# Kernel tuning notes

Hardware: AMD Instinct MI355X
Metric: run time of the kernel (lower is better)

Reference implementation:

```python
import jax, jax.numpy as jnp
import numpy as np

D_MODEL = 256
N_HEADS = 8
D_K = D_MODEL // N_HEADS
D_HID = D_MODEL // 2
LN_EPS = 1e-5


def setup_inputs() -> dict:
    key = jax.random.key(0)
    ks = jax.random.split(key, 16)
    B, ND, NT = 4, 512, 512
    s = 1.0 / np.sqrt(D_MODEL)
    inp = {
        'detections': jax.random.normal(ks[0], (B, ND, D_MODEL), jnp.float32),
        'tracks': jax.random.normal(ks[1], (B, NT, D_MODEL), jnp.float32),
        # attention projections, torch Linear convention: W [out, in], y = x W^T + b
        'w_q': jax.random.normal(ks[2], (D_MODEL, D_MODEL), jnp.float32) * s,
        'b_q': jnp.zeros((D_MODEL,), jnp.float32),
        'w_k': jax.random.normal(ks[3], (D_MODEL, D_MODEL), jnp.float32) * s,
        'b_k': jnp.zeros((D_MODEL,), jnp.float32),
        'w_v': jax.random.normal(ks[4], (D_MODEL, D_MODEL), jnp.float32) * s,
        'b_v': jnp.zeros((D_MODEL,), jnp.float32),
        'w_o': jax.random.normal(ks[5], (D_MODEL, D_MODEL), jnp.float32) * s,
        'b_o': jnp.zeros((D_MODEL,), jnp.float32),
        # LayerNorm
        'ln_g': jnp.ones((D_MODEL,), jnp.float32),
        'ln_b': jnp.zeros((D_MODEL,), jnp.float32),
        # association head MLP
        'w1': jax.random.normal(ks[6], (D_HID, D_MODEL), jnp.float32) * s,
        'b1': jnp.zeros((D_HID,), jnp.float32),
        'w2': jax.random.normal(ks[7], (1, D_HID), jnp.float32) * (1.0 / np.sqrt(D_HID)),
        'b2': jnp.zeros((1,), jnp.float32),
    }
    return inp


def _forward(detections, tracks, w_q, b_q, w_k, b_k, w_v, b_v, w_o, b_o,
             ln_g, ln_b, w1, b1, w2, b2):
    B, ND, D = detections.shape
    NT = tracks.shape[1]
    # cross-attention: query=detections, key=value=tracks
    Q = (detections @ w_q.T + b_q).reshape(B, ND, N_HEADS, D_K).transpose(0, 2, 1, 3)
    K = (tracks @ w_k.T + b_k).reshape(B, NT, N_HEADS, D_K).transpose(0, 2, 1, 3)
    V = (tracks @ w_v.T + b_v).reshape(B, NT, N_HEADS, D_K).transpose(0, 2, 1, 3)
    scores = jnp.einsum('bhqd,bhkd->bhqk', Q, K) / np.sqrt(D_K)
    attn = jax.nn.softmax(scores, axis=-1)
    ctx = jnp.einsum('bhqk,bhkd->bhqd', attn, V)  # [B,H,ND,D_K]
    ctx = ctx.transpose(0, 2, 1, 3).reshape(B, ND, D)
    attended = ctx @ w_o.T + b_o
    # residual + LayerNorm (dropout = identity in eval)
    x = detections + attended
    mu = jnp.mean(x, axis=-1, keepdims=True)
    var = jnp.var(x, axis=-1, keepdims=True)
    xn = (x - mu) * jax.lax.rsqrt(var + LN_EPS) * ln_g + ln_b
    # pairwise broadcast-multiply + 2-layer MLP + sigmoid
    combined = xn[:, :, None, :] * tracks[:, None, :, :]  # [B,ND,NT,D]
    h = jax.nn.relu(jnp.einsum('bntd,hd->bnth', combined, w1) + b1)
    logits = jnp.einsum('bnth,oh->bnto', h, w2) + b2  # [B,ND,NT,1]
    return jax.nn.sigmoid(logits[..., 0])


def reference(detections, tracks, w_q, b_q, w_k, b_k, w_v, b_v, w_o, b_o,
              ln_g, ln_b, w1, b1, w2, b2):
    return _forward(detections, tracks, w_q, b_q, w_k, b_k, w_v, b_v, w_o, b_o,
                    ln_g, ln_b, w1, b1, w2, b2)
```

## Files before the change

### kernel.cpp

```cpp
#include <hip/hip_runtime.h>

typedef _Float16 half8 __attribute__((ext_vector_type(8)));
typedef _Float16 half4v __attribute__((ext_vector_type(4)));
typedef _Float16 half2v __attribute__((ext_vector_type(2)));
typedef float f32x4 __attribute__((ext_vector_type(4)));

struct CvtJobs {
    const float* src[7];
    _Float16* dst[7];
    int n[7];
};

__global__ __launch_bounds__(256) void cvt_kernel(CvtJobs j) {
    int job = blockIdx.y;
    const float* s = j.src[job];
    _Float16* d = j.dst[job];
    int n = j.n[job];
    for (int i = blockIdx.x * blockDim.x + threadIdx.x; i < n;
         i += gridDim.x * blockDim.x)
        d[i] = (_Float16)s[i];
}

template<int MODE>
__global__ __launch_bounds__(256) void gemm_tn(
    const _Float16* __restrict__ A, const _Float16* __restrict__ Bm,
    _Float16* __restrict__ Ch, float* __restrict__ Cf,
    const float* __restrict__ bias, float alpha,
    int M, int N, int K, int lda, int ldb, int ldc)
{
    __shared__ _Float16 As[64][40];
    __shared__ _Float16 Bs[64][40];

    int tid = threadIdx.x;
    int l = tid & 63, w = tid >> 6;
    int wm = (w >> 1) * 32, wn = (w & 1) * 32;
    int m0 = blockIdx.x * 64, n0 = blockIdx.y * 64;
    int lr = tid >> 2, lc = (tid & 3) * 8;
    int ko = (l >> 4) * 8;

    f32x4 acc[2][2]{};

    for (int k0 = 0; k0 < K; k0 += 32) {
        half8 av = *(const half8*)(A + (long)(m0 + lr) * lda + k0 + lc);
        half8 bv = *(const half8*)(Bm + (long)(n0 + lr) * ldb + k0 + lc);
        __syncthreads();
        *(half8*)(&As[lr][lc]) = av;
        *(half8*)(&Bs[lr][lc]) = bv;
        __syncthreads();
        half8 a0 = *(const half8*)(&As[wm + (l & 15)][ko]);
        half8 a1 = *(const half8*)(&As[wm + 16 + (l & 15)][ko]);
        half8 b0 = *(const half8*)(&Bs[wn + (l & 15)][ko]);
        half8 b1 = *(const half8*)(&Bs[wn + 16 + (l & 15)][ko]);
        acc[0][0] = __builtin_amdgcn_mfma_f32_16x16x32_f16(a0, b0, acc[0][0], 0, 0, 0);
        acc[0][1] = __builtin_amdgcn_mfma_f32_16x16x32_f16(a0, b1, acc[0][1], 0, 0, 0);
        acc[1][0] = __builtin_amdgcn_mfma_f32_16x16x32_f16(a1, b0, acc[1][0], 0, 0, 0);
        acc[1][1] = __builtin_amdgcn_mfma_f32_16x16x32_f16(a1, b1, acc[1][1], 0, 0, 0);
    }

    #pragma unroll
    for (int mm = 0; mm < 2; ++mm)
    #pragma unroll
    for (int nn = 0; nn < 2; ++nn) {
        int row  = wm + mm * 16 + (l >> 4) * 4;
        int colg = n0 + wn + nn * 16 + (l & 15);
        float bc = bias ? bias[colg] : 0.f;
        if (MODE == 2) {
            half4v hv;
            #pragma unroll
            for (int i = 0; i < 4; ++i)
                hv[i] = (_Float16)(acc[mm][nn][i] * alpha + bc);
            int grow = m0 + row;
            int bb = grow >> 9, t = grow & 511;
            long off = ((long)(bb * 8 + (colg >> 5)) * 32 + (colg & 31)) * 512 + t;
            *(half4v*)(Ch + off) = hv;
        } else if (MODE == 0) {
            #pragma unroll
            for (int i = 0; i < 4; ++i)
                Ch[(long)(m0 + row + i) * ldc + colg] =
                    (_Float16)(acc[mm][nn][i] * alpha + bc);
        } else {
            #pragma unroll
            for (int i = 0; i < 4; ++i)
                Cf[(long)(m0 + row + i) * ldc + colg] =
                    acc[mm][nn][i] * alpha + bc;
        }
    }
}

__global__ __launch_bounds__(256) void flash_kernel(
    const _Float16* __restrict__ Q, const _Float16* __restrict__ K,
    const _Float16* __restrict__ vt, _Float16* __restrict__ ctx)
{
    __shared__ _Float16 P[4][16][264];
    int bh = blockIdx.y, b = bh >> 3, h = bh & 7;
    int q0 = blockIdx.x * 64;
    int tid = threadIdx.x, l = tid & 63, w = tid >> 6;
    int l15 = l & 15, g = l >> 4;

    const _Float16* qp = Q + ((long)b * 512 + q0 + w * 16 + l15) * 256 + h * 32 + g * 8;
    half8 qf = *(const half8*)qp;
    #pragma unroll
    for (int i = 0; i < 8; ++i) qf[i] = qf[i] * (_Float16)0.17677669529663687f;

    const _Float16* kp = K + ((long)b * 512 + l15) * 256 + h * 32 + g * 8;
    const _Float16* vp = vt + ((long)bh * 32 + l15) * 512 + g * 8;

    f32x4 c0{}, c1{};
    float m_run = -3e38f, sum_run = 0.f;
    f32x4 zero{};

    #pragma unroll
    for (int hf = 0; hf < 2; ++hf) {
        f32x4 s[16];
        #pragma unroll
        for (int t = 0; t < 16; ++t) {
            half8 kf = *(const half8*)(kp + (long)(hf * 16 + t) * (16 * 256));
            s[t] = __builtin_amdgcn_mfma_f32_16x16x32_f16(kf, qf, zero, 0, 0, 0);
        }
        float m0 = -3e38f, m1 = -3e38f, m2 = -3e38f, m3 = -3e38f;
        #pragma unroll
        for (int t = 0; t < 16; ++t) {
            m0 = fmaxf(m0, s[t][0]); m1 = fmaxf(m1, s[t][1]);
            m2 = fmaxf(m2, s[t][2]); m3 = fmaxf(m3, s[t][3]);
        }
        float ml = fmaxf(fmaxf(m0, m1), fmaxf(m2, m3));
        ml = fmaxf(ml, __shfl_xor(ml, 16, 64));
        ml = fmaxf(ml, __shfl_xor(ml, 32, 64));
        float m_new = fmaxf(m_run, ml);
        float scale = __expf(m_run - m_new);
        #pragma unroll
        for (int i = 0; i < 4; ++i) { c0[i] *= scale; c1[i] *= scale; }
        sum_run *= scale;
        float s0 = 0.f, s1 = 0.f, s2 = 0.f, s3 = 0.f;
        #pragma unroll
        for (int t = 0; t < 16; ++t) {
            s[t][0] = __expf(s[t][0] - m_new); s0 += s[t][0];
            s[t][1] = __expf(s[t][1] - m_new); s1 += s[t][1];
            s[t][2] = __expf(s[t][2] - m_new); s2 += s[t][2];
            s[t][3] = __expf(s[t][3] - m_new); s3 += s[t][3];
        }
        sum_run += (s0 + s1) + (s2 + s3);
        m_run = m_new;

        #pragma unroll
        for (int t = 0; t < 16; ++t) {
            half2v p01, p23;
            p01[0] = (_Float16)s[t][0]; p01[1] = (_Float16)s[t][1];
            p23[0] = (_Float16)s[t][2]; p23[1] = (_Float16)s[t][3];
            *(half2v*)&P[w][l15][t * 16 + g * 4]     = p01;
            *(half2v*)&P[w][l15][t * 16 + g * 4 + 2] = p23;
        }
        #pragma unroll
        for (int s2i = 0; s2i < 8; ++s2i) {
            half8 bf = *(const half8*)&P[w][l15][s2i * 32 + g * 8];
            half8 a0 = *(const half8*)(vp + hf * 256 + s2i * 32);
            half8 a1 = *(const half8*)(vp + 16 * 512 + hf * 256 + s2i * 32);
            c0 = __builtin_amdgcn_mfma_f32_16x16x32_f16(a0, bf, c0, 0, 0, 0);
            c1 = __builtin_amdgcn_mfma_f32_16x16x32_f16(a1, bf, c1, 0, 0, 0);
        }
    }
    sum_run += __shfl_xor(sum_run, 16, 64);
    sum_run += __shfl_xor(sum_run, 32, 64);
    float rs = 1.f / sum_run;
    _Float16* cp = ctx + ((long)b * 512 + q0 + w * 16 + l15) * 256 + h * 32;
    #pragma unroll
    for (int i = 0; i < 4; ++i) {
        cp[g * 4 + i]      = (_Float16)(c0[i] * rs);
        cp[16 + g * 4 + i] = (_Float16)(c1[i] * rs);
    }
}

__global__ __launch_bounds__(256) void ln_kernel(
    const float* __restrict__ det, const float* __restrict__ att,
    const float* __restrict__ g, const float* __restrict__ bta,
    _Float16* __restrict__ xn)
{
    int row = blockIdx.x, tid = threadIdx.x;
    long idx = (long)row * 256 + tid;
    float x = det[idx] + att[idx];
    float s1 = x, s2 = x * x;
    #pragma unroll
    for (int off = 32; off; off >>= 1) {
        s1 += __shfl_xor(s1, off, 64);
        s2 += __shfl_xor(s2, off, 64);
    }
    __shared__ float r1[4], r2[4];
    if ((tid & 63) == 0) { r1[tid >> 6] = s1; r2[tid >> 6] = s2; }
    __syncthreads();
    float S1 = r1[0] + r1[1] + r1[2] + r1[3];
    float S2 = r2[0] + r2[1] + r2[2] + r2[3];
    float mean = S1 * (1.f / 256.f);
    float var  = S2 * (1.f / 256.f) - mean * mean;
    float rsv = rsqrtf(var + 1e-5f);
    xn[idx] = (_Float16)((x - mean) * rsv * g[tid] + bta[tid]);
}

__global__ __launch_bounds__(256) void mlp_kernel(
    const _Float16* __restrict__ xn, const _Float16* __restrict__ trk,
    const _Float16* __restrict__ w1, const float* __restrict__ w2,
    const float* __restrict__ b1, const float* __restrict__ b2,
    float* __restrict__ out)
{
    int b  = blockIdx.z;
    int n0 = blockIdx.x * 32;
    int t0 = blockIdx.y * 32;
    int tid = threadIdx.x;
    int l = tid & 63, w = tid >> 6;
    int l15 = l & 15, g = l >> 4;
    int ko = g * 8;

    __shared__ _Float16 ts[32][264];
    __shared__ float part[4][32][33];

    {
        const _Float16* src = trk + ((long)b * 512 + t0) * 256;
        int r = tid >> 3, c0s = (tid & 7) * 8;
        #pragma unroll
        for (int c = 0; c < 256; c += 64)
            *(half8*)(&ts[r][c + c0s]) = *(const half8*)(src + r * 256 + c + c0s);
    }

    half8 wf[2][8];
    {
        const _Float16* w1p = w1 + (w * 32 + l15) * 256 + ko;
        #pragma unroll
        for (int a = 0; a < 2; ++a)
            #pragma unroll
            for (int ks = 0; ks < 8; ++ks)
                wf[a][ks] = *(const half8*)(w1p + a * 16 * 256 + ks * 32);
    }
    f32x4 binit[2]; f32x4 w2v[2];
    #pragma unroll
    for (int a = 0; a < 2; ++a)
        #pragma unroll
        for (int i = 0; i < 4; ++i) {
            int hh = w * 32 + a * 16 + g * 4 + i;
            binit[a][i] = b1[hh];
            w2v[a][i]   = w2[hh];
        }

    half8 bx[2][8];
    {
        const _Float16* xb = xn + ((long)b * 512 + n0 + l15) * 256 + ko;
        #pragma unroll
        for (int mm = 0; mm < 2; ++mm)
            #pragma unroll
            for (int ks = 0; ks < 8; ++ks)
                bx[mm][ks] = *(const half8*)(xb + mm * 16 * 256 + ks * 32);
    }

    __syncthreads();

    for (int tl = 0; tl < 32; ++tl) {
        f32x4 acc[2][2];
        #pragma unroll
        for (int a = 0; a < 2; ++a) {
            acc[a][0] = binit[a];
            acc[a][1] = binit[a];
        }
        #pragma unroll
        for (int ks = 0; ks < 8; ++ks) {
            half8 tf = *(const half8*)(&ts[tl][ks * 32 + ko]);
            half8 sa0 = wf[0][ks] * tf;
            half8 sa1 = wf[1][ks] * tf;
            acc[0][0] = __builtin_amdgcn_mfma_f32_16x16x32_f16(sa0, bx[0][ks], acc[0][0], 0, 0, 0);
            acc[0][1] = __builtin_amdgcn_mfma_f32_16x16x32_f16(sa0, bx[1][ks], acc[0][1], 0, 0, 0);
            acc[1][0] = __builtin_amdgcn_mfma_f32_16x16x32_f16(sa1, bx[0][ks], acc[1][0], 0, 0, 0);
            acc[1][1] = __builtin_amdgcn_mfma_f32_16x16x32_f16(sa1, bx[1][ks], acc[1][1], 0, 0, 0);
        }
        #pragma unroll
        for (int mm = 0; mm < 2; ++mm) {
            float x = 0.f;
            #pragma unroll
            for (int a = 0; a < 2; ++a)
                #pragma unroll
                for (int i = 0; i < 4; ++i)
                    x = fmaf(fmaxf(acc[a][mm][i], 0.f), w2v[a][i], x);
            x += __shfl_xor(x, 16, 64);
            x += __shfl_xor(x, 32, 64);
            if (g == 0) part[w][tl][mm * 16 + l15] = x;
        }
    }
    __syncthreads();

    float b2v = b2[0];
    int t = tid & 31;
    int nbase = tid >> 5;
    float* op = out + ((long)b * 512 + n0) * 512 + t0;
    #pragma unroll
    for (int k = 0; k < 4; ++k) {
        int nn = nbase + k * 8;
        float s = part[0][t][nn] + part[1][t][nn]
                + part[2][t][nn] + part[3][t][nn] + b2v;
        op[(long)nn * 512 + t] = 1.f / (1.f + __expf(-s));
    }
}

extern "C" void kernel_launch(void* const* d_in, const int* in_sizes, int n_in,
                              void* d_out, int out_size, void* d_ws, size_t ws_size,
                              hipStream_t stream)
{
    const float* det  = (const float*)d_in[0];
    const float* trk  = (const float*)d_in[1];
    const float* w_q  = (const float*)d_in[2];
    const float* b_q  = (const float*)d_in[3];
    const float* w_k  = (const float*)d_in[4];
    const float* b_k  = (const float*)d_in[5];
    const float* w_v  = (const float*)d_in[6];
    const float* b_v  = (const float*)d_in[7];
    const float* w_o  = (const float*)d_in[8];
    const float* b_o  = (const float*)d_in[9];
    const float* ln_g = (const float*)d_in[10];
    const float* ln_b = (const float*)d_in[11];
    const float* w1   = (const float*)d_in[12];
    const float* b1   = (const float*)d_in[13];
    const float* w2   = (const float*)d_in[14];
    const float* b2   = (const float*)d_in[15];
    float* out = (float*)d_out;

    char* ws = (char*)d_ws;
    const size_t O_DETH = 0;
    const size_t O_TRKH = O_DETH + (size_t)1048576;
    const size_t O_WQH  = O_TRKH + (size_t)1048576;
    const size_t O_WKH  = O_WQH + 131072;
    const size_t O_WVH  = O_WKH + 131072;
    const size_t O_WOH  = O_WVH + 131072;
    const size_t O_W1H  = O_WOH + 131072;
    const size_t O_QH   = O_W1H + 65536;
    const size_t O_KH   = O_QH + (size_t)1048576;
    const size_t O_VT   = O_KH + (size_t)1048576;
    const size_t O_CTXH = O_VT + (size_t)1048576;
    const size_t O_XNH  = O_CTXH + (size_t)1048576;
    const size_t O_ATT  = O_XNH + (size_t)1048576;

    _Float16* det_h  = (_Float16*)(ws + O_DETH);
    _Float16* trk_h  = (_Float16*)(ws + O_TRKH);
    _Float16* wq_h   = (_Float16*)(ws + O_WQH);
    _Float16* wk_h   = (_Float16*)(ws + O_WKH);
    _Float16* wv_h   = (_Float16*)(ws + O_WVH);
    _Float16* wo_h   = (_Float16*)(ws + O_WOH);
    _Float16* w1_h   = (_Float16*)(ws + O_W1H);
    _Float16* Q_h    = (_Float16*)(ws + O_QH);
    _Float16* K_h    = (_Float16*)(ws + O_KH);
    _Float16* vt     = (_Float16*)(ws + O_VT);
    _Float16* ctx_h  = (_Float16*)(ws + O_CTXH);
    _Float16* xn_h   = (_Float16*)(ws + O_XNH);
    float*    att_f  = (float*)(ws + O_ATT);

    CvtJobs cj;
    cj.src[0] = det; cj.dst[0] = det_h; cj.n[0] = 2048 * 256;
    cj.src[1] = trk; cj.dst[1] = trk_h; cj.n[1] = 2048 * 256;
    cj.src[2] = w_q; cj.dst[2] = wq_h;  cj.n[2] = 65536;
    cj.src[3] = w_k; cj.dst[3] = wk_h;  cj.n[3] = 65536;
    cj.src[4] = w_v; cj.dst[4] = wv_h;  cj.n[4] = 65536;
    cj.src[5] = w_o; cj.dst[5] = wo_h;  cj.n[5] = 65536;
    cj.src[6] = w1;  cj.dst[6] = w1_h;  cj.n[6] = 32768;
    cvt_kernel<<<dim3(512, 7), 256, 0, stream>>>(cj);

    gemm_tn<0><<<dim3(32, 4), 256, 0, stream>>>(det_h, wq_h, Q_h, nullptr, b_q, 1.f,
        2048, 256, 256, 256, 256, 256);
    gemm_tn<0><<<dim3(32, 4), 256, 0, stream>>>(trk_h, wk_h, K_h, nullptr, b_k, 1.f,
        2048, 256, 256, 256, 256, 256);
    gemm_tn<2><<<dim3(32, 4), 256, 0, stream>>>(trk_h, wv_h, vt, nullptr, b_v, 1.f,
        2048, 256, 256, 256, 256, 256);
    flash_kernel<<<dim3(8, 32), 256, 0, stream>>>(Q_h, K_h, vt, ctx_h);
    gemm_tn<1><<<dim3(32, 4), 256, 0, stream>>>(ctx_h, wo_h, nullptr, att_f, b_o, 1.f,
        2048, 256, 256, 256, 256, 256);
    ln_kernel<<<2048, 256, 0, stream>>>(det, att_f, ln_g, ln_b, xn_h);
    mlp_kernel<<<dim3(16, 16, 4), 256, 0, stream>>>(xn_h, trk_h, w1_h, w2, b1, b2, out);

    (void)in_sizes; (void)n_in; (void)out_size; (void)ws_size;
}
```

Baseline: 201.0 us.

## Fuse fp32→fp16 conversion into GEMMs, merge QKV, fuse out-proj with LayerNorm, 32x32 MFMA

Drops the standalone conversion kernel and converts fp32 inputs and weights to fp16 on the fly inside each consumer. The three QKV projections become a single launch over a z grid dimension. The output projection is fused with the residual add and LayerNorm, so the fp32 attention buffer round trip goes away. The MLP kernel moves to 32x32x16 MFMA tiles. Together these cut launch count and intermediate memory traffic, but the fused out-proj/LN kernel launches only 32 blocks, which may underuse the GPU.

```diff
diff --git a/kernel.cpp b/kernel.cpp
--- a/kernel.cpp
+++ b/kernel.cpp
@@ -4,57 +4,56 @@
 typedef _Float16 half4v __attribute__((ext_vector_type(4)));
 typedef _Float16 half2v __attribute__((ext_vector_type(2)));
 typedef float f32x4 __attribute__((ext_vector_type(4)));
-
-struct CvtJobs {
-    const float* src[7];
-    _Float16* dst[7];
-    int n[7];
-};
-
-__global__ __launch_bounds__(256) void cvt_kernel(CvtJobs j) {
-    int job = blockIdx.y;
-    const float* s = j.src[job];
-    _Float16* d = j.dst[job];
-    int n = j.n[job];
-    for (int i = blockIdx.x * blockDim.x + threadIdx.x; i < n;
-         i += gridDim.x * blockDim.x)
-        d[i] = (_Float16)s[i];
-}
-
-template<int MODE>
-__global__ __launch_bounds__(256) void gemm_tn(
-    const _Float16* __restrict__ A, const _Float16* __restrict__ Bm,
-    _Float16* __restrict__ Ch, float* __restrict__ Cf,
-    const float* __restrict__ bias, float alpha,
-    int M, int N, int K, int lda, int ldb, int ldc)
-{
+typedef float f32x16 __attribute__((ext_vector_type(16)));
+
+__device__ __forceinline__ half8 cvt8(const float4 a, const float4 b) {
+    half8 r;
+    r[0] = (_Float16)a.x; r[1] = (_Float16)a.y; r[2] = (_Float16)a.z; r[3] = (_Float16)a.w;
+    r[4] = (_Float16)b.x; r[5] = (_Float16)b.y; r[6] = (_Float16)b.z; r[7] = (_Float16)b.w;
+    return r;
+}
+
+__global__ __launch_bounds__(256) void qkv_kernel(
+    const float* __restrict__ det, const float* __restrict__ trk,
+    const float* __restrict__ wq, const float* __restrict__ wk,
+    const float* __restrict__ wv, const float* __restrict__ bq,
+    const float* __restrict__ bk, const float* __restrict__ bv,
+    _Float16* __restrict__ Qh, _Float16* __restrict__ Kh,
+    _Float16* __restrict__ vt)
+{
+    int z = blockIdx.z;
+    const float* A    = (z == 0) ? det : trk;
+    const float* Bm   = (z == 0) ? wq : (z == 1) ? wk : wv;
+    const float* bias = (z == 0) ? bq : (z == 1) ? bk : bv;
+
     __shared__ _Float16 As[64][40];
     __shared__ _Float16 Bs[64][40];
 
-    int tid = threadIdx.x;
-    int l = tid & 63, w = tid >> 6;
+    int tid = threadIdx.x, l = tid & 63, w = tid >> 6;
     int wm = (w >> 1) * 32, wn = (w & 1) * 32;
     int m0 = blockIdx.x * 64, n0 = blockIdx.y * 64;
     int lr = tid >> 2, lc = (tid & 3) * 8;
-    int ko = (l >> 4) * 8;
+    int ko = (l >> 4) * 8, l15 = l & 15;
 
     f32x4 acc[2][2]{};
 
-    for (int k0 = 0; k0 < K; k0 += 32) {
-        half8 av = *(const half8*)(A + (long)(m0 + lr) * lda + k0 + lc);
-        half8 bv = *(const half8*)(Bm + (long)(n0 + lr) * ldb + k0 + lc);
+    for (int k0 = 0; k0 < 256; k0 += 32) {
+        float4 a0 = *(const float4*)(A + (long)(m0 + lr) * 256 + k0 + lc);
+        float4 a1 = *(const float4*)(A + (long)(m0 + lr) * 256 + k0 + lc + 4);
+        float4 b0 = *(const float4*)(Bm + (long)(n0 + lr) * 256 + k0 + lc);
+        float4 b1 = *(const float4*)(Bm + (long)(n0 + lr) * 256 + k0 + lc + 4);
         __syncthreads();
-        *(half8*)(&As[lr][lc]) = av;
-        *(half8*)(&Bs[lr][lc]) = bv;
+        *(half8*)&As[lr][lc] = cvt8(a0, a1);
+        *(half8*)&Bs[lr][lc] = cvt8(b0, b1);
         __syncthreads();
-        half8 a0 = *(const half8*)(&As[wm + (l & 15)][ko]);
-        half8 a1 = *(const half8*)(&As[wm + 16 + (l & 15)][ko]);
-        half8 b0 = *(const half8*)(&Bs[wn + (l & 15)][ko]);
-        half8 b1 = *(const half8*)(&Bs[wn + 16 + (l & 15)][ko]);
-        acc[0][0] = __builtin_amdgcn_mfma_f32_16x16x32_f16(a0, b0, acc[0][0], 0, 0, 0);
-        acc[0][1] = __builtin_amdgcn_mfma_f32_16x16x32_f16(a0, b1, acc[0][1], 0, 0, 0);
-        acc[1][0] = __builtin_amdgcn_mfma_f32_16x16x32_f16(a1, b0, acc[1][0], 0, 0, 0);
-        acc[1][1] = __builtin_amdgcn_mfma_f32_16x16x32_f16(a1, b1, acc[1][1], 0, 0, 0);
+        half8 af0 = *(const half8*)(&As[wm + l15][ko]);
+        half8 af1 = *(const half8*)(&As[wm + 16 + l15][ko]);
+        half8 bf0 = *(const half8*)(&Bs[wn + l15][ko]);
+        half8 bf1 = *(const half8*)(&Bs[wn + 16 + l15][ko]);
+        acc[0][0] = __builtin_amdgcn_mfma_f32_16x16x32_f16(af0, bf0, acc[0][0], 0, 0, 0);
+        acc[0][1] = __builtin_amdgcn_mfma_f32_16x16x32_f16(af0, bf1, acc[0][1], 0, 0, 0);
+        acc[1][0] = __builtin_amdgcn_mfma_f32_16x16x32_f16(af1, bf0, acc[1][0], 0, 0, 0);
+        acc[1][1] = __builtin_amdgcn_mfma_f32_16x16x32_f16(af1, bf1, acc[1][1], 0, 0, 0);
     }
 
     #pragma unroll
@@ -62,27 +61,21 @@
     #pragma unroll
     for (int nn = 0; nn < 2; ++nn) {
         int row  = wm + mm * 16 + (l >> 4) * 4;
-        int colg = n0 + wn + nn * 16 + (l & 15);
-        float bc = bias ? bias[colg] : 0.f;
-        if (MODE == 2) {
+        int colg = n0 + wn + nn * 16 + l15;
+        float bc = bias[colg];
+        if (z == 2) {
             half4v hv;
             #pragma unroll
-            for (int i = 0; i < 4; ++i)
-                hv[i] = (_Float16)(acc[mm][nn][i] * alpha + bc);
+            for (int i = 0; i < 4; ++i) hv[i] = (_Float16)(acc[mm][nn][i] + bc);
             int grow = m0 + row;
             int bb = grow >> 9, t = grow & 511;
             long off = ((long)(bb * 8 + (colg >> 5)) * 32 + (colg & 31)) * 512 + t;
-            *(half4v*)(Ch + off) = hv;
-        } else if (MODE == 0) {
+            *(half4v*)(vt + off) = hv;
+        } else {
+            _Float16* C = (z == 0) ? Qh : Kh;
             #pragma unroll
             for (int i = 0; i < 4; ++i)
-                Ch[(long)(m0 + row + i) * ldc + colg] =
-                    (_Float16)(acc[mm][nn][i] * alpha + bc);
-        } else {
-            #pragma unroll
-            for (int i = 0; i < 4; ++i)
-                Cf[(long)(m0 + row + i) * ldc + colg] =
-                    acc[mm][nn][i] * alpha + bc;
+                C[(long)(m0 + row + i) * 256 + colg] = (_Float16)(acc[mm][nn][i] + bc);
         }
     }
 }
@@ -170,123 +163,169 @@
     }
 }
 
-__global__ __launch_bounds__(256) void ln_kernel(
-    const float* __restrict__ det, const float* __restrict__ att,
-    const float* __restrict__ g, const float* __restrict__ bta,
+__global__ __launch_bounds__(256) void outln_kernel(
+    const _Float16* __restrict__ ctx, const float* __restrict__ wo,
+    const float* __restrict__ bo, const float* __restrict__ det,
+    const float* __restrict__ lng, const float* __restrict__ lnb,
     _Float16* __restrict__ xn)
 {
-    int row = blockIdx.x, tid = threadIdx.x;
-    long idx = (long)row * 256 + tid;
-    float x = det[idx] + att[idx];
-    float s1 = x, s2 = x * x;
-    #pragma unroll
-    for (int off = 32; off; off >>= 1) {
-        s1 += __shfl_xor(s1, off, 64);
-        s2 += __shfl_xor(s2, off, 64);
-    }
-    __shared__ float r1[4], r2[4];
-    if ((tid & 63) == 0) { r1[tid >> 6] = s1; r2[tid >> 6] = s2; }
+    __shared__ _Float16 As[64][40];
+    __shared__ _Float16 Bs[256][40];
+    __shared__ float redS[4][64], redQ[4][64], mu[64], rsv[64];
+
+    int tid = threadIdx.x, l = tid & 63, w = tid >> 6;
+    int m0 = blockIdx.x * 64;
+    int wn = w * 64;
+    int lr = tid >> 2, lc = (tid & 3) * 8;
+    int ko = (l >> 4) * 8, l15 = l & 15, g4 = l >> 4;
+
+    f32x4 acc[4][4]{};
+
+    for (int k0 = 0; k0 < 256; k0 += 32) {
+        half8 av = *(const half8*)(ctx + (long)(m0 + lr) * 256 + k0 + lc);
+        float4 f[8];
+        #pragma unroll
+        for (int i = 0; i < 8; ++i)
+            f[i] = *(const float4*)(wo + (long)tid * 256 + k0 + i * 4);
+        __syncthreads();
+        *(half8*)&As[lr][lc] = av;
+        #pragma unroll
+        for (int i = 0; i < 4; ++i)
+            *(half8*)&Bs[tid][i * 8] = cvt8(f[2 * i], f[2 * i + 1]);
+        __syncthreads();
+        half8 afr[4], bfr[4];
+        #pragma unroll
+        for (int mm = 0; mm < 4; ++mm) afr[mm] = *(const half8*)&As[mm * 16 + l15][ko];
+        #pragma unroll
+        for (int nn = 0; nn < 4; ++nn) bfr[nn] = *(const half8*)&Bs[wn + nn * 16 + l15][ko];
+        #pragma unroll
+        for (int mm = 0; mm < 4; ++mm)
+            #pragma unroll
+            for (int nn = 0; nn < 4; ++nn)
+                acc[mm][nn] = __builtin_amdgcn_mfma_f32_16x16x32_f16(afr[mm], bfr[nn], acc[mm][nn], 0, 0, 0);
+    }
+
+    float bov[4], gv[4], bev[4];
+    #pragma unroll
+    for (int nn = 0; nn < 4; ++nn) {
+        int c = wn + nn * 16 + l15;
+        bov[nn] = bo[c]; gv[nn] = lng[c]; bev[nn] = lnb[c];
+    }
+    #pragma unroll
+    for (int mm = 0; mm < 4; ++mm)
+    #pragma unroll
+    for (int i = 0; i < 4; ++i) {
+        int r = mm * 16 + g4 * 4 + i;
+        float s = 0.f, q = 0.f;
+        #pragma unroll
+        for (int nn = 0; nn < 4; ++nn) {
+            float x = acc[mm][nn][i] + bov[nn]
+                    + det[(long)(m0 + r) * 256 + wn + nn * 16 + l15];
+            acc[mm][nn][i] = x;
+            s += x; q += x * x;
+        }
+        #pragma unroll
+        for (int off = 1; off < 16; off <<= 1) {
+            s += __shfl_xor(s, off, 64);
+            q += __shfl_xor(q, off, 64);
+        }
+        if (l15 == 0) { redS[w][r] = s; redQ[w][r] = q; }
+    }
     __syncthreads();
-    float S1 = r1[0] + r1[1] + r1[2] + r1[3];
-    float S2 = r2[0] + r2[1] + r2[2] + r2[3];
-    float mean = S1 * (1.f / 256.f);
-    float var  = S2 * (1.f / 256.f) - mean * mean;
-    float rsv = rsqrtf(var + 1e-5f);
-    xn[idx] = (_Float16)((x - mean) * rsv * g[tid] + bta[tid]);
+    if (tid < 64) {
+        float S = redS[0][tid] + redS[1][tid] + redS[2][tid] + redS[3][tid];
+        float Qs = redQ[0][tid] + redQ[1][tid] + redQ[2][tid] + redQ[3][tid];
+        float mean = S * (1.f / 256.f);
+        float var = Qs * (1.f / 256.f) - mean * mean;
+        mu[tid] = mean;
+        rsv[tid] = rsqrtf(var + 1e-5f);
+    }
+    __syncthreads();
+    #pragma unroll
+    for (int mm = 0; mm < 4; ++mm)
+    #pragma unroll
+    for (int i = 0; i < 4; ++i) {
+        int r = mm * 16 + g4 * 4 + i;
+        float mr = mu[r], rr = rsv[r];
+        #pragma unroll
+        for (int nn = 0; nn < 4; ++nn)
+            xn[(long)(m0 + r) * 256 + wn + nn * 16 + l15] =
+                (_Float16)((acc[mm][nn][i] - mr) * rr * gv[nn] + bev[nn]);
+    }
 }
 
 __global__ __launch_bounds__(256) void mlp_kernel(
-    const _Float16* __restrict__ xn, const _Float16* __restrict__ trk,
-    const _Float16* __restrict__ w1, const float* __restrict__ w2,
+    const _Float16* __restrict__ xn, const float* __restrict__ trk,
+    const float* __restrict__ w1, const float* __restrict__ w2,
     const float* __restrict__ b1, const float* __restrict__ b2,
     float* __restrict__ out)
 {
-    int b  = blockIdx.z;
-    int n0 = blockIdx.x * 32;
-    int t0 = blockIdx.y * 32;
-    int tid = threadIdx.x;
-    int l = tid & 63, w = tid >> 6;
-    int l15 = l & 15, g = l >> 4;
-    int ko = g * 8;
+    int b = blockIdx.z, n0g = blockIdx.x * 32, t0 = blockIdx.y * 32;
+    int tid = threadIdx.x, l = tid & 63, w = tid >> 6;
+    int l31 = l & 31, hk = (l >> 5) * 8;
 
     __shared__ _Float16 ts[32][264];
     __shared__ float part[4][32][33];
 
     {
-        const _Float16* src = trk + ((long)b * 512 + t0) * 256;
-        int r = tid >> 3, c0s = (tid & 7) * 8;
-        #pragma unroll
-        for (int c = 0; c < 256; c += 64)
-            *(half8*)(&ts[r][c + c0s]) = *(const half8*)(src + r * 256 + c + c0s);
-    }
-
-    half8 wf[2][8];
+        const float* src = trk + ((long)b * 512 + t0) * 256;
+        int r = tid >> 3, c0s = (tid & 7) * 32;
+        float4 f[8];
+        #pragma unroll
+        for (int i = 0; i < 8; ++i)
+            f[i] = *(const float4*)(src + (long)r * 256 + c0s + i * 4);
+        #pragma unroll
+        for (int i = 0; i < 4; ++i)
+            *(half8*)&ts[r][c0s + i * 8] = cvt8(f[2 * i], f[2 * i + 1]);
+    }
+
+    half8 wf[16];
     {
-        const _Float16* w1p = w1 + (w * 32 + l15) * 256 + ko;
-        #pragma unroll
-        for (int a = 0; a < 2; ++a)
-            #pragma unroll
-            for (int ks = 0; ks < 8; ++ks)
-                wf[a][ks] = *(const half8*)(w1p + a * 16 * 256 + ks * 32);
-    }
-    f32x4 binit[2]; f32x4 w2v[2];
-    #pragma unroll
-    for (int a = 0; a < 2; ++a)
-        #pragma unroll
-        for (int i = 0; i < 4; ++i) {
-            int hh = w * 32 + a * 16 + g * 4 + i;
-            binit[a][i] = b1[hh];
-            w2v[a][i]   = w2[hh];
-        }
-
-    half8 bx[2][8];
+        const float* wp = w1 + (long)(w * 32 + l31) * 256 + hk;
+        #pragma unroll
+        for (int ks = 0; ks < 16; ++ks) {
+            float4 fa = *(const float4*)(wp + ks * 16);
+            float4 fb = *(const float4*)(wp + ks * 16 + 4);
+            wf[ks] = cvt8(fa, fb);
+        }
+    }
+    half8 bx[16];
     {
-        const _Float16* xb = xn + ((long)b * 512 + n0 + l15) * 256 + ko;
-        #pragma unroll
-        for (int mm = 0; mm < 2; ++mm)
-            #pragma unroll
-            for (int ks = 0; ks < 8; ++ks)
-                bx[mm][ks] = *(const half8*)(xb + mm * 16 * 256 + ks * 32);
+        const _Float16* xb = xn + ((long)b * 512 + n0g + l31) * 256 + hk;
+        #pragma unroll
+        for (int ks = 0; ks < 16; ++ks)
+            bx[ks] = *(const half8*)(xb + ks * 16);
+    }
+    f32x16 binit, w2v;
+    #pragma unroll
+    for (int r = 0; r < 16; ++r) {
+        int hh = w * 32 + (r & 3) + 8 * (r >> 2) + 4 * (l >> 5);
+        binit[r] = b1[hh];
+        w2v[r]  = w2[hh];
     }
 
     __syncthreads();
 
     for (int tl = 0; tl < 32; ++tl) {
-        f32x4 acc[2][2];
-        #pragma unroll
-        for (int a = 0; a < 2; ++a) {
-            acc[a][0] = binit[a];
-            acc[a][1] = binit[a];
-        }
-        #pragma unroll
-        for (int ks = 0; ks < 8; ++ks) {
-            half8 tf = *(const half8*)(&ts[tl][ks * 32 + ko]);
-            half8 sa0 = wf[0][ks] * tf;
-            half8 sa1 = wf[1][ks] * tf;
-            acc[0][0] = __builtin_amdgcn_mfma_f32_16x16x32_f16(sa0, bx[0][ks], acc[0][0], 0, 0, 0);
-            acc[0][1] = __builtin_amdgcn_mfma_f32_16x16x32_f16(sa0, bx[1][ks], acc[0][1], 0, 0, 0);
-            acc[1][0] = __builtin_amdgcn_mfma_f32_16x16x32_f16(sa1, bx[0][ks], acc[1][0], 0, 0, 0);
-            acc[1][1] = __builtin_amdgcn_mfma_f32_16x16x32_f16(sa1, bx[1][ks], acc[1][1], 0, 0, 0);
-        }
-        #pragma unroll
-        for (int mm = 0; mm < 2; ++mm) {
-            float x = 0.f;
-            #pragma unroll
-            for (int a = 0; a < 2; ++a)
-                #pragma unroll
-                for (int i = 0; i < 4; ++i)
-                    x = fmaf(fmaxf(acc[a][mm][i], 0.f), w2v[a][i], x);
-            x += __shfl_xor(x, 16, 64);
-            x += __shfl_xor(x, 32, 64);
-            if (g == 0) part[w][tl][mm * 16 + l15] = x;
-        }
+        f32x16 acc = binit;
+        #pragma unroll
+        for (int ks = 0; ks < 16; ++ks) {
+            half8 tf = *(const half8*)&ts[tl][ks * 16 + hk];
+            half8 sa = wf[ks] * tf;
+            acc = __builtin_amdgcn_mfma_f32_32x32x16_f16(sa, bx[ks], acc, 0, 0, 0);
+        }
+        float x = 0.f;
+        #pragma unroll
+        for (int r = 0; r < 16; ++r)
+            x = fmaf(fmaxf(acc[r], 0.f), w2v[r], x);
+        x += __shfl_xor(x, 32, 64);
+        if (l < 32) part[w][tl][l] = x;
     }
     __syncthreads();
 
     float b2v = b2[0];
-    int t = tid & 31;
-    int nbase = tid >> 5;
-    float* op = out + ((long)b * 512 + n0) * 512 + t0;
+    int t = tid & 31, nbase = tid >> 5;
+    float* op = out + ((long)b * 512 + n0g) * 512 + t0;
     #pragma unroll
     for (int k = 0; k < 4; ++k) {
         int nn = nbase + k * 8;
@@ -319,55 +358,17 @@
     float* out = (float*)d_out;
 
     char* ws = (char*)d_ws;
-    const size_t O_DETH = 0;
-    const size_t O_TRKH = O_DETH + (size_t)1048576;
-    const size_t O_WQH  = O_TRKH + (size_t)1048576;
-    const size_t O_WKH  = O_WQH + 131072;
-    const size_t O_WVH  = O_WKH + 131072;
-    const size_t O_WOH  = O_WVH + 131072;
-    const size_t O_W1H  = O_WOH + 131072;
-    const size_t O_QH   = O_W1H + 65536;
-    const size_t O_KH   = O_QH + (size_t)1048576;
-    const size_t O_VT   = O_KH + (size_t)1048576;
-    const size_t O_CTXH = O_VT + (size_t)1048576;
-    const size_t O_XNH  = O_CTXH + (size_t)1048576;
-    const size_t O_ATT  = O_XNH + (size_t)1048576;
-
-    _Float16* det_h  = (_Float16*)(ws + O_DETH);
-    _Float16* trk_h  = (_Float16*)(ws + O_TRKH);
-    _Float16* wq_h   = (_Float16*)(ws + O_WQH);
-    _Float16* wk_h   = (_Float16*)(ws + O_WKH);
-    _Float16* wv_h   = (_Float16*)(ws + O_WVH);
-    _Float16* wo_h   = (_Float16*)(ws + O_WOH);
-    _Float16* w1_h   = (_Float16*)(ws + O_W1H);
-    _Float16* Q_h    = (_Float16*)(ws + O_QH);
-    _Float16* K_h    = (_Float16*)(ws + O_KH);
-    _Float16* vt     = (_Float16*)(ws + O_VT);
-    _Float16* ctx_h  = (_Float16*)(ws + O_CTXH);
-    _Float16* xn_h   = (_Float16*)(ws + O_XNH);
-    float*    att_f  = (float*)(ws + O_ATT);
-
-    CvtJobs cj;
-    cj.src[0] = det; cj.dst[0] = det_h; cj.n[0] = 2048 * 256;
-    cj.src[1] = trk; cj.dst[1] = trk_h; cj.n[1] = 2048 * 256;
-    cj.src[2] = w_q; cj.dst[2] = wq_h;  cj.n[2] = 65536;
-    cj.src[3] = w_k; cj.dst[3] = wk_h;  cj.n[3] = 65536;
-    cj.src[4] = w_v; cj.dst[4] = wv_h;  cj.n[4] = 65536;
-    cj.src[5] = w_o; cj.dst[5] = wo_h;  cj.n[5] = 65536;
-    cj.src[6] = w1;  cj.dst[6] = w1_h;  cj.n[6] = 32768;
-    cvt_kernel<<<dim3(512, 7), 256, 0, stream>>>(cj);
-
-    gemm_tn<0><<<dim3(32, 4), 256, 0, stream>>>(det_h, wq_h, Q_h, nullptr, b_q, 1.f,
-        2048, 256, 256, 256, 256, 256);
-    gemm_tn<0><<<dim3(32, 4), 256, 0, stream>>>(trk_h, wk_h, K_h, nullptr, b_k, 1.f,
-        2048, 256, 256, 256, 256, 256);
-    gemm_tn<2><<<dim3(32, 4), 256, 0, stream>>>(trk_h, wv_h, vt, nullptr, b_v, 1.f,
-        2048, 256, 256, 256, 256, 256);
+    _Float16* Q_h   = (_Float16*)(ws);
+    _Float16* K_h   = (_Float16*)(ws + (size_t)1048576);
+    _Float16* vt    = (_Float16*)(ws + (size_t)2097152);
+    _Float16* ctx_h = (_Float16*)(ws + (size_t)3145728);
+    _Float16* xn_h  = (_Float16*)(ws + (size_t)4194304);
+
+    qkv_kernel<<<dim3(32, 4, 3), 256, 0, stream>>>(
+        det, trk, w_q, w_k, w_v, b_q, b_k, b_v, Q_h, K_h, vt);
     flash_kernel<<<dim3(8, 32), 256, 0, stream>>>(Q_h, K_h, vt, ctx_h);
-    gemm_tn<1><<<dim3(32, 4), 256, 0, stream>>>(ctx_h, wo_h, nullptr, att_f, b_o, 1.f,
-        2048, 256, 256, 256, 256, 256);
-    ln_kernel<<<2048, 256, 0, stream>>>(det, att_f, ln_g, ln_b, xn_h);
-    mlp_kernel<<<dim3(16, 16, 4), 256, 0, stream>>>(xn_h, trk_h, w1_h, w2, b1, b2, out);
+    outln_kernel<<<32, 256, 0, stream>>>(ctx_h, w_o, b_o, det, ln_g, ln_b, xn_h);
+    mlp_kernel<<<dim3(16, 16, 4), 256, 0, stream>>>(xn_h, trk, w1, w2, b1, b2, out);
 
     (void)in_sizes; (void)n_in; (void)out_size; (void)ws_size;
 }
```

Measured after the change: 208.1 us. 1.04x slower.
